# Kernel tuning notes

Hardware: AMD Instinct MI355X
Metric: run time of the kernel (lower is better)

## Reference

```python
import jax, jax.numpy as jnp
import numpy as np

CODEBOOK_SIZE = 1024
EMBEDDING_DIM = 256
COMMITMENT_COST = 0.25


def setup_inputs() -> dict:
    key = jax.random.key(0)
    k1, k2 = jax.random.split(key)
    x = jax.random.normal(k1, (32, EMBEDDING_DIM, 32, 32), dtype=jnp.float32)
    # embedding initialized uniform(-1/K, 1/K) like the torch module
    embedding = jax.random.uniform(
        k2, (CODEBOOK_SIZE, EMBEDDING_DIM), dtype=jnp.float32,
        minval=-1.0 / CODEBOOK_SIZE, maxval=1.0 / CODEBOOK_SIZE)
    return {"x": x, "embedding": embedding}


def reference(x, embedding):
    # x: [B, C, H, W] -> inputs: [B, H, W, C]
    inputs = jnp.transpose(x, (0, 2, 3, 1))
    input_shape = inputs.shape
    flat = inputs.reshape(-1, EMBEDDING_DIM)  # [N, D]
    # squared L2 distances to codebook: [N, K]
    distances = (jnp.sum(flat ** 2, axis=1, keepdims=True)
                 + jnp.sum(embedding ** 2, axis=1)
                 - 2.0 * flat @ embedding.T)
    encoding_indices = jnp.argmin(distances, axis=1)  # [N]
    encodings = jax.nn.one_hot(encoding_indices, CODEBOOK_SIZE, dtype=jnp.float32)  # [N, K]
    # gather (same math as encodings @ embedding)
    quantized = embedding[encoding_indices].reshape(input_shape)  # [B, H, W, C]
    e_latent_loss = jnp.mean((jax.lax.stop_gradient(quantized) - inputs) ** 2)
    q_latent_loss = jnp.mean((quantized - jax.lax.stop_gradient(inputs)) ** 2)
    loss = q_latent_loss + COMMITMENT_COST * e_latent_loss
    # straight-through estimator
    quantized_st = inputs + jax.lax.stop_gradient(quantized - inputs)
    return (loss, jnp.transpose(quantized_st, (0, 3, 1, 2)), encodings)
```

## Files before the change

kernel.cpp:

```cpp
#include <hip/hip_runtime.h>
#include <cstdint>
#include <cstddef>

constexpr int B = 32, C = 256, H = 32, W = 32;
constexpr int NPTS = B * H * W;
constexpr int DIM  = 256;
constexpr int K    = 1024;
constexpr int QELEMS = B * C * H * W;
constexpr int CHW = C * H * W;

typedef __attribute__((ext_vector_type(8))) short s8v;
typedef __attribute__((ext_vector_type(4))) float f32x4;

#define GLD_LDS16(g, l)                                                        \
  __builtin_amdgcn_global_load_lds(                                            \
      (const __attribute__((address_space(1))) unsigned int*)(g),              \
      (__attribute__((address_space(3))) unsigned int*)(l), 16, 0, 0)

__device__ __forceinline__ unsigned short f2bf(float f) {
  unsigned u = __float_as_uint(f);
  return (unsigned short)((u + 0x7FFFu + ((u >> 16) & 1u)) >> 16);
}

__global__ __launch_bounds__(256) void prep_kernel(
    const float* __restrict__ x, const float* __restrict__ emb,
    unsigned short* __restrict__ ehi, float* __restrict__ esq,
    unsigned short* __restrict__ xhi, float* __restrict__ xsq) {
  __shared__ float xls[DIM][32];
  const int t = threadIdx.x;
  const int bid = blockIdx.x;

  if (bid < 16) {
    float (*sums)[64] = (float (*)[64])xls;
    const int k = bid * 64 + (t & 63);
    const int seg = t >> 6;
    const float* er = emb + (size_t)k * DIM + seg * 64;
    float v[64];
    float4* v4 = (float4*)v;
#pragma unroll
    for (int i = 0; i < 16; ++i) v4[i] = *(const float4*)(er + i * 4);
    float s = 0.f;
#pragma unroll
    for (int i = 0; i < 64; ++i) s = fmaf(v[i], v[i], s);
    unsigned short* eo = ehi + (size_t)k * DIM + seg * 64;
#pragma unroll
    for (int i = 0; i < 8; ++i) {
      unsigned short h[8];
#pragma unroll
      for (int j = 0; j < 8; ++j) h[j] = f2bf(v[i * 8 + j]);
      *(s8v*)(eo + i * 8) = *(s8v*)h;
    }
    sums[seg][t & 63] = s;
    __syncthreads();
    if (t < 64)
      esq[bid * 64 + t] =
          ((sums[0][t] + sums[1][t]) + sums[2][t]) + sums[3][t];
    return;
  }

  const int n0 = (bid - 16) * 32;
  const int bb = n0 >> 10, hw0 = n0 & 1023;
  const float* xb = x + (size_t)bb * CHW + hw0;
  const int lane = t & 63, w = t >> 6;
  const int row_off = lane >> 3;
  const int p4 = (lane & 7) * 4;
#pragma unroll
  for (int i = 0; i < 8; ++i) {
    const int c0 = w * 64 + i * 8;
    GLD_LDS16(xb + (size_t)(c0 + row_off) * 1024 + p4, &xls[c0][0]);
  }
  __syncthreads();

  if (t < 32) {
    float s = 0.f;
#pragma unroll 8
    for (int c = 0; c < 256; ++c) {
      const float v = xls[c][t];
      s = fmaf(v, v, s);
    }
    xsq[n0 + t] = s;
  }
  const int p2 = t & 31, cb = (t >> 5) * 32;
  unsigned short* xo = xhi + (size_t)(n0 + p2) * DIM + cb;
#pragma unroll
  for (int i = 0; i < 4; ++i) {
    unsigned short h[8];
#pragma unroll
    for (int j = 0; j < 8; ++j) h[j] = f2bf(xls[cb + i * 8 + j][p2]);
    *(s8v*)(xo + i * 8) = *(s8v*)h;
  }
}

constexpr float MARGIN = 1e-3f;
__global__ __launch_bounds__(256) void coarse_kernel(
    const unsigned short* __restrict__ xhi, const unsigned short* __restrict__ ehi,
    const float* __restrict__ esq, const float* __restrict__ xsq,
    float* __restrict__ part, unsigned int* __restrict__ cand) {
  __shared__ __align__(16) unsigned short xs[128][32];
  __shared__ __align__(16) unsigned short es[128][32];
  __shared__ float xsq_s[128], esq_s[128], thr_s[128];
  __shared__ unsigned long long red2[2][128];
  __shared__ unsigned int cntL[128];

  const int t = threadIdx.x;
  const int lane = t & 63, w = t >> 6;
  const int wn = (w & 1) * 64, wk = (w >> 1) * 64;
  const int col = lane & 15, quad = lane >> 4;
  const int nblk = blockIdx.x * 128;
  const int kblk = blockIdx.y * 128;

  if (t < 128) {
    xsq_s[t] = xsq[nblk + t];
    esq_s[t] = esq[kblk + t];
    cntL[t] = 0u;
  }

  f32x4 acc[4][4];
#pragma unroll
  for (int i = 0; i < 4; ++i)
#pragma unroll
    for (int j = 0; j < 4; ++j) acc[i][j] = (f32x4){0.f, 0.f, 0.f, 0.f};

  const int gl_row = lane >> 2;
  const int gl_c   = (lane & 3) * 8;

  for (int c0 = 0; c0 < DIM; c0 += 32) {
    __syncthreads();
#pragma unroll
    for (int i = 0; i < 2; ++i) {
      const int inst = w + 4 * i;
      const int row = inst * 16 + gl_row;
      GLD_LDS16(xhi + (size_t)(nblk + row) * DIM + c0 + gl_c, &xs[inst * 16][0]);
      GLD_LDS16(ehi + (size_t)(kblk + row) * DIM + c0 + gl_c, &es[inst * 16][0]);
    }
    __syncthreads();
    s8v a[4], b[4];
#pragma unroll
    for (int ti = 0; ti < 4; ++ti)
      a[ti] = *(const s8v*)&xs[wn + ti * 16 + col][quad * 8];
#pragma unroll
    for (int tj = 0; tj < 4; ++tj)
      b[tj] = *(const s8v*)&es[wk + tj * 16 + col][quad * 8];
#pragma unroll
    for (int ti = 0; ti < 4; ++ti)
#pragma unroll
      for (int tj = 0; tj < 4; ++tj)
        acc[ti][tj] = __builtin_amdgcn_mfma_f32_16x16x32_bf16(
            a[ti], b[tj], acc[ti][tj], 0, 0, 0);
  }

  unsigned long long nmin[4][4];
#pragma unroll
  for (int ti = 0; ti < 4; ++ti)
#pragma unroll
    for (int r = 0; r < 4; ++r) nmin[ti][r] = ~0ULL;
#pragma unroll
  for (int ti = 0; ti < 4; ++ti)
#pragma unroll
    for (int tj = 0; tj < 4; ++tj) {
      const int krel = wk + tj * 16 + col;
      const float eq = esq_s[krel];
#pragma unroll
      for (int r = 0; r < 4; ++r) {
        const int nl = wn + ti * 16 + quad * 4 + r;
        const float d = (xsq_s[nl] + eq) - 2.f * acc[ti][tj][r];
        const unsigned long long key =
            ((unsigned long long)__float_as_uint(d) << 32) |
            (unsigned)(kblk + krel);
        if (key < nmin[ti][r]) nmin[ti][r] = key;
      }
    }
#pragma unroll
  for (int o = 1; o < 16; o <<= 1)
#pragma unroll
    for (int ti = 0; ti < 4; ++ti)
#pragma unroll
      for (int r = 0; r < 4; ++r) {
        const unsigned long long v = __shfl_xor(nmin[ti][r], o, 64);
        if (v < nmin[ti][r]) nmin[ti][r] = v;
      }
  if (col == 0) {
#pragma unroll
    for (int ti = 0; ti < 4; ++ti)
#pragma unroll
      for (int r = 0; r < 4; ++r)
        red2[w >> 1][wn + ti * 16 + quad * 4 + r] = nmin[ti][r];
  }
  __syncthreads();
  if (t < 128) {
    const unsigned long long m0 = red2[0][t], m1 = red2[1][t];
    const unsigned long long m = (m1 < m0) ? m1 : m0;
    const float dmin = __uint_as_float((unsigned)(m >> 32));
    part[(size_t)(nblk + t) * 8 + blockIdx.y] = dmin;
    thr_s[t] = dmin + MARGIN;
  }
  __syncthreads();
#pragma unroll
  for (int ti = 0; ti < 4; ++ti)
#pragma unroll
    for (int tj = 0; tj < 4; ++tj) {
      const int krel = wk + tj * 16 + col;
      const float eq = esq_s[krel];
#pragma unroll
      for (int r = 0; r < 4; ++r) {
        const int nl = wn + ti * 16 + quad * 4 + r;
        const float d = (xsq_s[nl] + eq) - 2.f * acc[ti][tj][r];
        if (d <= thr_s[nl]) {
          const unsigned slot = atomicAdd(&cntL[nl], 1u);
          if (slot < 4u)
            cand[((size_t)(nblk + nl) * 8 + blockIdx.y) * 4 + slot] =
                (unsigned)(kblk + krel);
        }
      }
    }
  __syncthreads();
  if (t < 128) {
    unsigned c = cntL[t];
    const size_t base = ((size_t)(nblk + t) * 8 + blockIdx.y) * 4;
    if (c > 4u) { cand[base + 3] = 0xFFFFFFFEu; c = 3u; }
    for (unsigned s = c; s < 4u; ++s) cand[base + s] = 0xFFFFFFFFu;
  }
}

__global__ __launch_bounds__(256) void finish2_kernel(
    const float* __restrict__ x, const float* __restrict__ emb,
    const float* __restrict__ esq, const float* __restrict__ xsq,
    const float* __restrict__ part, const unsigned int* __restrict__ cand,
    float* __restrict__ outq, float* __restrict__ enc,
    float* __restrict__ lws) {
  __shared__ __align__(16) float xls[DIM][33];
  __shared__ unsigned list[1024];
  __shared__ unsigned rlist[256];
  __shared__ unsigned long long best[32];
  __shared__ float thr_s[32];
  __shared__ float xsq_s[32];
  __shared__ int ids_s[32];
  __shared__ int lcnt, rcnt;

  const int t = threadIdx.x;
  const int n0 = blockIdx.x * 32;
  const int bb = n0 >> 10, hw0 = n0 & 1023;

  const float* xb = x + (size_t)bb * CHW + hw0;
  {
    const int p = t & 31, cs = t >> 5;
#pragma unroll 8
    for (int r = 0; r < 32; ++r) {
      const int c = r * 8 + cs;
      xls[c][p] = xb[(size_t)c * 1024 + p];
    }
  }
  if (t == 0) { lcnt = 0; rcnt = 0; }
  if (t < 32) {
    best[t] = ~0ULL;
    xsq_s[t] = xsq[n0 + t];
    const float4 p0 = *(const float4*)&part[(size_t)(n0 + t) * 8];
    const float4 p1 = *(const float4*)&part[(size_t)(n0 + t) * 8 + 4];
    float g = fminf(fminf(fminf(p0.x, p0.y), fminf(p0.z, p0.w)),
                    fminf(fminf(p1.x, p1.y), fminf(p1.z, p1.w)));
    thr_s[t] = g + MARGIN;
  }
  __syncthreads();

  {
    const int nn = t >> 3, s = t & 7;
    const float pv = part[(size_t)(n0 + nn) * 8 + s];
    if (pv <= thr_s[nn]) {
      const uint4 c4 = *(const uint4*)&cand[((size_t)(n0 + nn) * 8 + s) * 4];
      if (c4.w == 0xFFFFFFFEu) {
        const int rp = atomicAdd(&rcnt, 1);
        if (rp < 256) rlist[rp] = ((unsigned)nn << 3) | (unsigned)s;
      } else {
        const unsigned vs[4] = {c4.x, c4.y, c4.z, c4.w};
#pragma unroll
        for (int i = 0; i < 4; ++i) {
          const unsigned v = vs[i];
          if (v <= 1023u) {
            const int pos = atomicAdd(&lcnt, 1);
            if (pos < 1024) list[pos] = ((unsigned)nn << 11) | v;
          }
        }
      }
    }
  }
  __syncthreads();

  const int L = lcnt < 1024 ? lcnt : 1024;
  for (int e = t; e < L; e += 256) {
    const unsigned entry = list[e];
    const int p = entry >> 11;
    const int k = entry & 2047;
    const float xq = xsq_s[p];
    const float* er = emb + (size_t)k * DIM;
    float dot = 0.f;
#pragma unroll 4
    for (int c4 = 0; c4 < DIM; c4 += 4) {
      const float4 e4 = *(const float4*)(er + c4);
      dot = fmaf(xls[c4 + 0][p], e4.x, dot);
      dot = fmaf(xls[c4 + 1][p], e4.y, dot);
      dot = fmaf(xls[c4 + 2][p], e4.z, dot);
      dot = fmaf(xls[c4 + 3][p], e4.w, dot);
    }
    const float t1 = xq + esq[k];
    const float d = t1 - 2.f * dot;
    const unsigned long long key =
        ((unsigned long long)__float_as_uint(d) << 32) | (unsigned)k;
    atomicMin(&best[p], key);
  }

  const int R = rcnt < 256 ? rcnt : 256;
  for (int rb = 0; rb < R; rb += 2) {
    const int ri = rb + (t >> 7);
    if (ri < R) {
      const unsigned rs = rlist[ri];
      const int p = rs >> 3;
      const int k = (int)(rs & 7u) * 128 + (t & 127);
      const float xq = xsq_s[p];
      const float* er = emb + (size_t)k * DIM;
      float dot = 0.f;
#pragma unroll 4
      for (int c4 = 0; c4 < DIM; c4 += 4) {
        const float4 e4 = *(const float4*)(er + c4);
        dot = fmaf(xls[c4 + 0][p], e4.x, dot);
        dot = fmaf(xls[c4 + 1][p], e4.y, dot);
        dot = fmaf(xls[c4 + 2][p], e4.z, dot);
        dot = fmaf(xls[c4 + 3][p], e4.w, dot);
      }
      const float t1 = xq + esq[k];
      const float d = t1 - 2.f * dot;
      const unsigned long long key =
          ((unsigned long long)__float_as_uint(d) << 32) | (unsigned)k;
      atomicMin(&best[p], key);
    }
  }
  __syncthreads();

  if (t < 32) {
    ids_s[t] = (int)(best[t] & 0xFFFFFFFFu);
    float s = __uint_as_float((unsigned)(best[t] >> 32));
#pragma unroll
    for (int o = 16; o > 0; o >>= 1) s += __shfl_down(s, o, 64);
    if (t == 0) lws[blockIdx.x] = s;
  }
  __syncthreads();

  {
    float* sl = enc + (size_t)n0 * K;
    float* b4 = sl + 3;
#pragma unroll
    for (int j = 0; j < 32; ++j) {
      const int idx = t + j * 256;
      if (idx < 8191) {
        const int lf = 3 + 4 * idx;
        float4 v;
        v.x = (((lf + 0) & 1023) == ids_s[(lf + 0) >> 10]) ? 1.f : 0.f;
        v.y = (((lf + 1) & 1023) == ids_s[(lf + 1) >> 10]) ? 1.f : 0.f;
        v.z = (((lf + 2) & 1023) == ids_s[(lf + 2) >> 10]) ? 1.f : 0.f;
        v.w = (((lf + 3) & 1023) == ids_s[(lf + 3) >> 10]) ? 1.f : 0.f;
        *(float4*)(b4 + 4 * idx) = v;
      }
    }
    if (t == 0) {
      sl[0] = (ids_s[0] == 0) ? 1.f : 0.f;
      sl[1] = (ids_s[0] == 1) ? 1.f : 0.f;
      sl[2] = (ids_s[0] == 2) ? 1.f : 0.f;
      sl[32767] = (ids_s[31] == 1023) ? 1.f : 0.f;
    }
  }

  {
    const int p = t & 31, g = t >> 5;
    const int row = ids_s[p];
    const float* er = emb + (size_t)row * DIM + g * 32;
    float* ob = outq + (size_t)bb * CHW + hw0 + p;
#pragma unroll
    for (int i = 0; i < 8; ++i) {
      const float4 v = *(const float4*)(er + i * 4);
      const int c = g * 32 + i * 4;
      ob[(size_t)(c + 0) * 1024] = v.x;
      ob[(size_t)(c + 1) * 1024] = v.y;
      ob[(size_t)(c + 2) * 1024] = v.z;
      ob[(size_t)(c + 3) * 1024] = v.w;
    }
  }
}

__global__ __launch_bounds__(256) void loss_reduce(
    const float* __restrict__ lws, float* __restrict__ loss) {
  __shared__ float red[4];
  const int t = threadIdx.x;
  float s = 0.f;
#pragma unroll
  for (int i = 0; i < 4; ++i) s += lws[t + i * 256];
#pragma unroll
  for (int o = 32; o > 0; o >>= 1) s += __shfl_down(s, o, 64);
  if ((t & 63) == 0) red[t >> 6] = s;
  __syncthreads();
  if (t == 0)
    *loss = (((red[0] + red[1]) + red[2]) + red[3]) * (1.25f / (float)QELEMS);
}

extern "C" void kernel_launch(void* const* d_in, const int* in_sizes, int n_in,
                              void* d_out, int out_size, void* d_ws, size_t ws_size,
                              hipStream_t stream) {
  const float* x   = (const float*)d_in[0];
  const float* emb = (const float*)d_in[1];
  float* out  = (float*)d_out;
  float* loss = out;
  float* outq = out + 1;
  float* enc  = out + 1 + QELEMS;

  char* ws = (char*)d_ws;
  unsigned short* ehi  = (unsigned short*)ws;
  float*          esq  = (float*)(ws + 524288);
  float*          xsq  = (float*)(ws + 528384);
  float*          part = (float*)(ws + 659456);
  unsigned int*   cand = (unsigned int*)(ws + 1708032);
  unsigned short* xhi  = (unsigned short*)(ws + 5902336);
  float*          lws  = (float*)(ws + 22679552);

  prep_kernel<<<16 + 1024, 256, 0, stream>>>(x, emb, ehi, esq, xhi, xsq);
  dim3 cg(NPTS / 128, 8);
  coarse_kernel<<<cg, 256, 0, stream>>>(xhi, ehi, esq, xsq, part, cand);
  finish2_kernel<<<NPTS / 32, 256, 0, stream>>>(x, emb, esq, xsq, part, cand,
                                                outq, enc, lws);
  loss_reduce<<<1, 256, 0, stream>>>(lws, loss);
}
```

Before: 283.0 us.

## Split output writing into separate kernel with memset-based one-hot encoding

The resolve kernel now only computes the nearest-code indices and writes them to a workspace buffer. A new kernel scatters 1.0 into a one-hot buffer that hipMemsetAsync has already zeroed, and writes the quantized output row-wise with coalesced vector stores by gathering embedding columns. The goal is to move the 128MB one-hot write onto the fill engine and take it off the argmin kernel. The cost is an extra kernel launch and a strided gather from the embedding table.

```diff
diff --git a/kernel.cpp b/kernel.cpp
--- a/kernel.cpp
+++ b/kernel.cpp
@@ -222,19 +222,17 @@
   }
 }
 
-__global__ __launch_bounds__(256) void finish2_kernel(
+__global__ __launch_bounds__(256) void resolve_kernel(
     const float* __restrict__ x, const float* __restrict__ emb,
     const float* __restrict__ esq, const float* __restrict__ xsq,
     const float* __restrict__ part, const unsigned int* __restrict__ cand,
-    float* __restrict__ outq, float* __restrict__ enc,
-    float* __restrict__ lws) {
+    int* __restrict__ ids_g, float* __restrict__ lws) {
   __shared__ __align__(16) float xls[DIM][33];
   __shared__ unsigned list[1024];
   __shared__ unsigned rlist[256];
   __shared__ unsigned long long best[32];
   __shared__ float thr_s[32];
   __shared__ float xsq_s[32];
-  __shared__ int ids_s[32];
   __shared__ int lcnt, rcnt;
 
   const int t = threadIdx.x;
@@ -336,51 +334,51 @@
   __syncthreads();
 
   if (t < 32) {
-    ids_s[t] = (int)(best[t] & 0xFFFFFFFFu);
+    ids_g[n0 + t] = (int)(best[t] & 0xFFFFFFFFu);
     float s = __uint_as_float((unsigned)(best[t] >> 32));
 #pragma unroll
     for (int o = 16; o > 0; o >>= 1) s += __shfl_down(s, o, 64);
     if (t == 0) lws[blockIdx.x] = s;
   }
-  __syncthreads();
-
-  {
-    float* sl = enc + (size_t)n0 * K;
-    float* b4 = sl + 3;
-#pragma unroll
-    for (int j = 0; j < 32; ++j) {
-      const int idx = t + j * 256;
-      if (idx < 8191) {
-        const int lf = 3 + 4 * idx;
-        float4 v;
-        v.x = (((lf + 0) & 1023) == ids_s[(lf + 0) >> 10]) ? 1.f : 0.f;
-        v.y = (((lf + 1) & 1023) == ids_s[(lf + 1) >> 10]) ? 1.f : 0.f;
-        v.z = (((lf + 2) & 1023) == ids_s[(lf + 2) >> 10]) ? 1.f : 0.f;
-        v.w = (((lf + 3) & 1023) == ids_s[(lf + 3) >> 10]) ? 1.f : 0.f;
-        *(float4*)(b4 + 4 * idx) = v;
-      }
-    }
-    if (t == 0) {
-      sl[0] = (ids_s[0] == 0) ? 1.f : 0.f;
-      sl[1] = (ids_s[0] == 1) ? 1.f : 0.f;
-      sl[2] = (ids_s[0] == 2) ? 1.f : 0.f;
-      sl[32767] = (ids_s[31] == 1023) ? 1.f : 0.f;
-    }
-  }
-
-  {
-    const int p = t & 31, g = t >> 5;
-    const int row = ids_s[p];
-    const float* er = emb + (size_t)row * DIM + g * 32;
-    float* ob = outq + (size_t)bb * CHW + hw0 + p;
-#pragma unroll
-    for (int i = 0; i < 8; ++i) {
-      const float4 v = *(const float4*)(er + i * 4);
-      const int c = g * 32 + i * 4;
-      ob[(size_t)(c + 0) * 1024] = v.x;
-      ob[(size_t)(c + 1) * 1024] = v.y;
-      ob[(size_t)(c + 2) * 1024] = v.z;
-      ob[(size_t)(c + 3) * 1024] = v.w;
+}
+
+__global__ __launch_bounds__(256) void onesq_kernel(
+    const float* __restrict__ emb, const int* __restrict__ ids_g,
+    float* __restrict__ outq, float* __restrict__ enc) {
+  __shared__ int ids_s[1024];
+  const int t = threadIdx.x;
+  const int b = blockIdx.x >> 6;
+  const int cg = blockIdx.x & 63;
+#pragma unroll
+  for (int i = 0; i < 4; ++i)
+    ids_s[t + i * 256] = ids_g[b * 1024 + t + i * 256];
+  __syncthreads();
+
+  if (cg == 0) {
+#pragma unroll
+    for (int i = 0; i < 4; ++i) {
+      const int p = t + i * 256;
+      enc[(size_t)(b * 1024 + p) * K + ids_s[p]] = 1.0f;
+    }
+  }
+
+#pragma unroll
+  for (int r = 0; r < 4; ++r) {
+    const int c = cg * 4 + r;
+    float* row = outq + (size_t)(b * 256 + c) * 1024;
+    if (t < 255) {
+      const int f = 3 + 4 * t;
+      f32x4 v;
+      v.x = emb[(size_t)ids_s[f + 0] * DIM + c];
+      v.y = emb[(size_t)ids_s[f + 1] * DIM + c];
+      v.z = emb[(size_t)ids_s[f + 2] * DIM + c];
+      v.w = emb[(size_t)ids_s[f + 3] * DIM + c];
+      *(f32x4*)(row + f) = v;
+    } else {
+      row[0] = emb[(size_t)ids_s[0] * DIM + c];
+      row[1] = emb[(size_t)ids_s[1] * DIM + c];
+      row[2] = emb[(size_t)ids_s[2] * DIM + c];
+      row[1023] = emb[(size_t)ids_s[1023] * DIM + c];
     }
   }
 }
@@ -418,11 +416,15 @@
   unsigned int*   cand = (unsigned int*)(ws + 1708032);
   unsigned short* xhi  = (unsigned short*)(ws + 5902336);
   float*          lws  = (float*)(ws + 22679552);
+  int*            ids  = (int*)(ws + 22683648);
+
+  hipMemsetAsync(enc, 0, (size_t)NPTS * K * sizeof(float), stream);
 
   prep_kernel<<<16 + 1024, 256, 0, stream>>>(x, emb, ehi, esq, xhi, xsq);
   dim3 cg(NPTS / 128, 8);
   coarse_kernel<<<cg, 256, 0, stream>>>(xhi, ehi, esq, xsq, part, cand);
-  finish2_kernel<<<NPTS / 32, 256, 0, stream>>>(x, emb, esq, xsq, part, cand,
-                                                outq, enc, lws);
+  resolve_kernel<<<NPTS / 32, 256, 0, stream>>>(x, emb, esq, xsq, part, cand,
+                                                ids, lws);
+  onesq_kernel<<<2048, 256, 0, stream>>>(emb, ids, outq, enc);
   loss_reduce<<<1, 256, 0, stream>>>(lws, loss);
 }
```

New measurement: 306.4 us. 8.3% more time.
